# Kernel optimization log

Hardware: AMD Instinct MI355X
Metric: run time of the kernel (lower is better)

## Reference

```python
import jax, jax.numpy as jnp
import numpy as np

HEAD_SIZE = 128
EMBED_DIM = 1024
BLOCK = 2048


def setup_inputs() -> dict:
    key = jax.random.key(0)
    kx, kk, kq, kv = jax.random.split(key, 4)
    x = jax.random.normal(kx, (8, BLOCK, EMBED_DIM), dtype=jnp.float32)
    # nn.Linear weights stored as [out, in]; apply as x @ W.T -> keep as [in, out]
    s = 1.0 / np.sqrt(EMBED_DIM)
    W_key = jax.random.uniform(kk, (EMBED_DIM, HEAD_SIZE), jnp.float32, -s, s)
    W_query = jax.random.uniform(kq, (EMBED_DIM, HEAD_SIZE), jnp.float32, -s, s)
    W_value = jax.random.uniform(kv, (EMBED_DIM, HEAD_SIZE), jnp.float32, -s, s)
    return {"x": x, "W_key": W_key, "W_query": W_query, "W_value": W_value}


def reference(x, W_key, W_query, W_value):
    # NOTE: faithful to the source bug: q = self.key(x), W_query is unused.
    B, T, C = x.shape
    k = x @ W_key          # [B, T, H]
    q = x @ W_key          # [B, T, H]  (source uses key() for q too)
    scores = jnp.einsum("bqh,bkh->bqk", q, k) * (HEAD_SIZE ** -0.5)
    causal = jnp.tril(jnp.ones((T, T), dtype=bool))
    scores = jnp.where(causal, scores, -jnp.inf)
    weights = jax.nn.softmax(scores, axis=-1)
    v = x @ W_value        # [B, T, H]
    out = jnp.einsum("bqk,bkh->bqh", weights, v)
    return out
```

## Files before the change

kernel.cpp:

```cpp
#include <hip/hip_runtime.h>
#include <hip/hip_bf16.h>

typedef __attribute__((ext_vector_type(8))) short bf16x8;
typedef __attribute__((ext_vector_type(4))) short bf16x4;
typedef __attribute__((ext_vector_type(4))) float f32x4;

#define HS 128
#define ED 1024
#define TT 2048
#define NBATCH 8
#define NROWS (NBATCH * TT)
#define CHUNKS 4
#define TPC 8

__device__ __forceinline__ short bf16rne(float f) {
    unsigned u = __builtin_bit_cast(unsigned, f);
    u = u + 0x7fffu + ((u >> 16) & 1u);
    return (short)(u >> 16);
}

__device__ __forceinline__ void gl_lds16(const void* g, void* l) {
    __builtin_amdgcn_global_load_lds(
        (const __attribute__((address_space(1))) unsigned int*)g,
        (__attribute__((address_space(3))) unsigned int*)l, 16, 0, 0);
}

template <int NCALLS, int RBL2>
__device__ __forceinline__ void stage_tile(const char* gbase, void* lds,
                                           int gpitch, int tid, int wv) {
#pragma unroll
    for (int c = 0; c < NCALLS; ++c) {
        const int o = c * 4096 + tid * 16;
        const int row = o >> RBL2;
        const int colU = (o & ((1 << RBL2) - 1)) ^ ((row & 7) << 4);
        const char* g = gbase + (size_t)row * gpitch + colU;
        char* l = (char*)lds + c * 4096 + wv * 1024;
        gl_lds16(g, l);
    }
}

__device__ __forceinline__ bf16x8 lds_rd7(const short* lds, int row, int colE) {
    const int o = (row << 7) + (((colE * 2) & 127) ^ ((row & 7) << 4));
    return *reinterpret_cast<const bf16x8*>((const char*)lds + o);
}
__device__ __forceinline__ bf16x8 lds_rd8(const short* lds, int row, int colE) {
    const int o = (row << 8) + (((colE * 2) & 255) ^ ((row & 7) << 4));
    return *reinterpret_cast<const bf16x8*>((const char*)lds + o);
}

__global__ void k_wtrans(const float* __restrict__ Wk, const float* __restrict__ Wv,
                         short* __restrict__ WkT, short* __restrict__ WvT) {
    const float* W = blockIdx.y ? Wv : Wk;
    short* WT = blockIdx.y ? WvT : WkT;
    __shared__ float tile[16][128];
    const int k0 = blockIdx.x * 16;
    const int t = threadIdx.x;
#pragma unroll
    for (int i = 0; i < 8; ++i) {
        int idx = t + i * 256;
        tile[idx >> 7][idx & 127] = W[(size_t)(k0 + (idx >> 7)) * HS + (idx & 127)];
    }
    __syncthreads();
    const int n = t >> 1;
    const int h = (t & 1) * 8;
    bf16x8 o;
#pragma unroll
    for (int i = 0; i < 8; ++i) o[i] = bf16rne(tile[h + i][n]);
    *reinterpret_cast<bf16x8*>(&WT[(size_t)n * ED + k0 + h]) = o;
}

__global__ __launch_bounds__(256) void k_proj(
        const float* __restrict__ x,
        const short* __restrict__ WkT, const short* __restrict__ WvT,
        short* __restrict__ Kbuf, short* __restrict__ VT) {
    __shared__ short xl[2][64 * 64];
    __shared__ short wl[2][128 * 64];

    const int tid = threadIdx.x;
    const int lane = tid & 63;
    const int wv = tid >> 6;
    const int lr = lane & 15, g = lane >> 4;
    const int side = blockIdx.x;
    const int r0 = blockIdx.y * 64;
    const short* WT = side ? WvT : WkT;

    f32x4 acc[8];
#pragma unroll
    for (int i = 0; i < 8; ++i) acc[i] = (f32x4){0.f, 0.f, 0.f, 0.f};

    int xo[2], xrow[2], xcolU[2];
#pragma unroll
    for (int j = 0; j < 2; ++j) {
        xo[j] = tid * 32 + j * 16;
        xrow[j] = xo[j] >> 7;
        xcolU[j] = (xo[j] & 127) ^ ((xrow[j] & 7) << 4);
    }
    f32x4 xr[2][2][2];

#define XLOAD(s, set)                                                                \
    {                                                                                \
        _Pragma("unroll") for (int j = 0; j < 2; ++j) {                              \
            const float* sp = x + (size_t)(r0 + xrow[j]) * ED + (s) * 64 + (xcolU[j] >> 1); \
            xr[set][j][0] = *reinterpret_cast<const f32x4*>(sp);                     \
            xr[set][j][1] = *reinterpret_cast<const f32x4*>(sp + 4);                 \
        }                                                                            \
    }
#define XWRITE(set, buf)                                                             \
    {                                                                                \
        _Pragma("unroll") for (int j = 0; j < 2; ++j) {                              \
            bf16x8 pk;                                                               \
            _Pragma("unroll") for (int i = 0; i < 8; ++i)                            \
                pk[i] = bf16rne(xr[set][j][i >> 2][i & 3]);                          \
            *reinterpret_cast<bf16x8*>((char*)&xl[buf][0] + xo[j]) = pk;             \
        }                                                                            \
    }

    XLOAD(0, 0);
    XLOAD(1, 1);
    stage_tile<4, 7>((const char*)WT, &wl[0][0], ED * 2, tid, wv);
    XWRITE(0, 0);
    __syncthreads();

#pragma unroll
    for (int s = 0; s < 16; ++s) {
        const int cur = s & 1;
        if (s + 1 < 16) {
            stage_tile<4, 7>((const char*)WT + (size_t)(s + 1) * 128, &wl[cur ^ 1][0],
                             ED * 2, tid, wv);
            XWRITE((s + 1) & 1, cur ^ 1);
        }
        if (s + 2 < 16) XLOAD(s + 2, cur);
        bf16x8 af[2];
#pragma unroll
        for (int ks = 0; ks < 2; ++ks)
            af[ks] = lds_rd7(&xl[cur][0], wv * 16 + lr, ks * 32 + g * 8);
#pragma unroll
        for (int ks = 0; ks < 2; ++ks)
#pragma unroll
            for (int nf = 0; nf < 8; ++nf) {
                bf16x8 bfr = lds_rd7(&wl[cur][0], nf * 16 + lr, ks * 32 + g * 8);
                acc[nf] = __builtin_amdgcn_mfma_f32_16x16x32_bf16(af[ks], bfr, acc[nf], 0, 0, 0);
            }
        __syncthreads();
    }
#undef XLOAD
#undef XWRITE

    const int mb = r0 + wv * 16 + 4 * g;
    if (side == 0) {
#pragma unroll
        for (int nf = 0; nf < 8; ++nf) {
            const int n = nf * 16 + lr;
#pragma unroll
            for (int r = 0; r < 4; ++r)
                Kbuf[(size_t)(mb + r) * HS + n] = bf16rne(acc[nf][r]);
        }
    } else {
        const int b = mb >> 11, tt = mb & (TT - 1);
#pragma unroll
        for (int nf = 0; nf < 8; ++nf) {
            const int n = nf * 16 + lr;
            bf16x4 o;
#pragma unroll
            for (int r = 0; r < 4; ++r) o[r] = bf16rne(acc[nf][r]);
            *reinterpret_cast<bf16x4*>(&VT[((size_t)b * HS + n) * TT + tt]) = o;
        }
    }
}

__global__ __launch_bounds__(256) void k_attn(
        const short* __restrict__ Kbuf, const short* __restrict__ VT,
        float* __restrict__ Opart, float* __restrict__ ml) {
    __shared__ short kl[2][64 * 128];
    __shared__ short vl[2][128 * 64];
    __shared__ short plds[4][16][72];

    const int tid = threadIdx.x;
    const int lane = tid & 63;
    const int wv = tid >> 6;
    const int lr = lane & 15, g = lane >> 4;

    const int bid = blockIdx.x;
    const int b = bid & 7;
    const int w = bid >> 3;
    int c, qt;
    if (w < 32)      { c = 0; qt = 31 - w; }
    else if (w < 56) { c = 1; qt = 31 - (w - 32); }
    else if (w < 72) { c = 2; qt = 31 - (w - 56); }
    else             { c = 3; qt = 31 - (w - 72); }
    const int t_begin = c * TPC;
    const int t_end = min(t_begin + TPC, qt + 1);

    const short* Kb = Kbuf + (size_t)b * TT * HS;
    const short* Vb = VT + (size_t)b * HS * TT;
    const int q0 = qt * 64 + wv * 16;

    bf16x8 qf[4];
#pragma unroll
    for (int ks = 0; ks < 4; ++ks)
        qf[ks] = *reinterpret_cast<const bf16x8*>(&Kb[(size_t)(q0 + lr) * HS + ks * 32 + g * 8]);

    stage_tile<4, 8>((const char*)(Kb + (size_t)t_begin * 64 * HS), &kl[0][0], HS * 2, tid, wv);
    stage_tile<4, 7>((const char*)(Vb + t_begin * 64), &vl[0][0], TT * 2, tid, wv);
    __syncthreads();

    float mrun = -1e30f, lrun = 0.f;
    f32x4 oacc[8];
#pragma unroll
    for (int i = 0; i < 8; ++i) oacc[i] = (f32x4){0.f, 0.f, 0.f, 0.f};

    const float c1 = 0.08838834764831845f * 1.4426950408889634f;
    const int qrow = q0 + lr;
    int cur = 0;

    for (int t = t_begin; t < t_end; ++t) {
        const int kv0 = t * 64;
        if (t + 1 < t_end) {
            stage_tile<4, 8>((const char*)(Kb + (size_t)(kv0 + 64) * HS), &kl[cur ^ 1][0],
                             HS * 2, tid, wv);
            stage_tile<4, 7>((const char*)(Vb + kv0 + 64), &vl[cur ^ 1][0], TT * 2, tid, wv);
        }

        f32x4 s[4];
#pragma unroll
        for (int i = 0; i < 4; ++i) s[i] = (f32x4){0.f, 0.f, 0.f, 0.f};
        __builtin_amdgcn_s_setprio(1);
#pragma unroll
        for (int ks = 0; ks < 4; ++ks) {
            bf16x8 kf[4];
#pragma unroll
            for (int mf = 0; mf < 4; ++mf)
                kf[mf] = lds_rd8(&kl[cur][0], mf * 16 + lr, ks * 32 + g * 8);
#pragma unroll
            for (int mf = 0; mf < 4; ++mf)
                s[mf] = __builtin_amdgcn_mfma_f32_16x16x32_bf16(kf[mf], qf[ks], s[mf], 0, 0, 0);
        }
        __builtin_amdgcn_s_setprio(0);

        float pv[4][4];
        float tmax = -1e30f;
#pragma unroll
        for (int mf = 0; mf < 4; ++mf)
#pragma unroll
            for (int r = 0; r < 4; ++r) {
                const int kv = kv0 + mf * 16 + 4 * g + r;
                float v = s[mf][r] * c1;
                v = (kv <= qrow) ? v : -1e30f;
                pv[mf][r] = v;
                tmax = fmaxf(tmax, v);
            }
        tmax = fmaxf(tmax, __shfl_xor(tmax, 16));
        tmax = fmaxf(tmax, __shfl_xor(tmax, 32));
        const float mnew = fmaxf(mrun, tmax);
        const float alpha = exp2f(mrun - mnew);
        mrun = mnew;
        float tsum = 0.f;
#pragma unroll
        for (int mf = 0; mf < 4; ++mf)
#pragma unroll
            for (int r = 0; r < 4; ++r) {
                const float p = exp2f(pv[mf][r] - mnew);
                pv[mf][r] = p;
                tsum += p;
            }
        tsum += __shfl_xor(tsum, 16);
        tsum += __shfl_xor(tsum, 32);
        lrun = lrun * alpha + tsum;
#pragma unroll
        for (int i = 0; i < 8; ++i) oacc[i] *= alpha;

#pragma unroll
        for (int mf = 0; mf < 4; ++mf) {
            bf16x4 pk;
#pragma unroll
            for (int r = 0; r < 4; ++r) pk[r] = bf16rne(pv[mf][r]);
            *reinterpret_cast<bf16x4*>(&plds[wv][lr][mf * 16 + g * 4]) = pk;
        }
        __builtin_amdgcn_s_setprio(1);
#pragma unroll
        for (int ks = 0; ks < 2; ++ks) {
            bf16x8 pf = *reinterpret_cast<const bf16x8*>(&plds[wv][lr][ks * 32 + g * 8]);
            bf16x8 vf[8];
#pragma unroll
            for (int mf = 0; mf < 8; ++mf)
                vf[mf] = lds_rd7(&vl[cur][0], mf * 16 + lr, ks * 32 + g * 8);
#pragma unroll
            for (int mf = 0; mf < 8; ++mf)
                oacc[mf] = __builtin_amdgcn_mfma_f32_16x16x32_bf16(vf[mf], pf, oacc[mf], 0, 0, 0);
        }
        __builtin_amdgcn_s_setprio(0);

        __syncthreads();
        cur ^= 1;
    }

    const int row = b * TT + q0 + lr;
    const size_t pidx = (size_t)c * NROWS + row;
    float* op = Opart + pidx * HS;
#pragma unroll
    for (int mf = 0; mf < 8; ++mf)
        *reinterpret_cast<f32x4*>(&op[mf * 16 + g * 4]) = oacc[mf];
    if (lane < 16) {
        ml[pidx * 2] = mrun;
        ml[pidx * 2 + 1] = lrun;
    }
}

__global__ __launch_bounds__(256) void k_merge(const float* __restrict__ Opart,
                                               const float* __restrict__ ml,
                                               float* __restrict__ out) {
    const int idx = blockIdx.x * 256 + threadIdx.x;
    const int row = idx >> 5;
    const int h4 = (idx & 31) * 4;
    const int qt64 = (row & (TT - 1)) >> 6;
    const int nvalid = (qt64 >> 3) + 1;
    float m[CHUNKS], l[CHUNKS];
    float M = -1e30f;
#pragma unroll
    for (int c = 0; c < CHUNKS; ++c) {
        const bool valid = c < nvalid;
        const size_t p = (size_t)c * NROWS + row;
        m[c] = valid ? ml[p * 2] : -1e30f;
        l[c] = valid ? ml[p * 2 + 1] : 0.f;
        M = fmaxf(M, m[c]);
    }
    float denom = 0.f;
    f32x4 o = (f32x4){0.f, 0.f, 0.f, 0.f};
#pragma unroll
    for (int c = 0; c < CHUNKS; ++c) {
        const bool valid = c < nvalid;
        const float wgt = valid ? exp2f(m[c] - M) : 0.f;
        denom += wgt * l[c];
        if (valid) {
            f32x4 p = *reinterpret_cast<const f32x4*>(
                &Opart[((size_t)c * NROWS + row) * HS + h4]);
            o += p * wgt;
        }
    }
    const float inv = 1.0f / denom;
    *reinterpret_cast<f32x4*>(&out[(size_t)row * HS + h4]) = o * inv;
}

extern "C" void kernel_launch(void* const* d_in, const int* in_sizes, int n_in,
                              void* d_out, int out_size, void* d_ws, size_t ws_size,
                              hipStream_t stream) {
    (void)in_sizes; (void)n_in; (void)out_size; (void)ws_size;
    const float* x  = (const float*)d_in[0];
    const float* Wk = (const float*)d_in[1];
    const float* Wv = (const float*)d_in[3];
    float* out = (float*)d_out;

    char* ws = (char*)d_ws;
    short* Kbuf = (short*)ws;
    short* VT   = (short*)(ws + (size_t)NROWS * HS * 2);
    short* WkT  = (short*)(ws + 2 * (size_t)NROWS * HS * 2);
    short* WvT  = WkT + (size_t)HS * ED;
    float* Opart = (float*)(WvT + (size_t)HS * ED);
    float* mlb   = Opart + (size_t)CHUNKS * NROWS * HS;

    hipLaunchKernelGGL(k_wtrans, dim3(64, 2), dim3(256), 0, stream, Wk, Wv, WkT, WvT);
    hipLaunchKernelGGL(k_proj, dim3(2, NROWS / 64), dim3(256), 0, stream, x, WkT, WvT, Kbuf, VT);
    hipLaunchKernelGGL(k_attn, dim3(640), dim3(256), 0, stream, Kbuf, VT, Opart, mlb);
    hipLaunchKernelGGL(k_merge, dim3(NROWS * 32 / 256), dim3(256), 0, stream, Opart, mlb, out);
}
```

Measured before the change: 165.3 us.

## Replace full syncthreads with partial vmcnt waits to keep prefetches in flight

Swaps __syncthreads in the projection and attention loops for explicit s_waitcnt vmcnt(N) plus s_barrier, so the next tile's global-to-LDS loads can stay outstanding while the current tile is computed. The projection loop moves the X register-to-LDS write after the MFMA block, and the attention loop issues the next K/V stage at the top of each iteration, then waits only for the current tile. This relies on hand-counted outstanding memory operations and on the compiler's ordering, so a wrong count would race.

```diff
diff --git a/kernel.cpp b/kernel.cpp
--- a/kernel.cpp
+++ b/kernel.cpp
@@ -17,6 +17,17 @@
     unsigned u = __builtin_bit_cast(unsigned, f);
     u = u + 0x7fffu + ((u >> 16) & 1u);
     return (short)(u >> 16);
+}
+
+template <int N>
+__device__ __forceinline__ void vmwait() {
+    if constexpr (N == 0)      asm volatile("s_waitcnt vmcnt(0)" ::: "memory");
+    else if constexpr (N == 4) asm volatile("s_waitcnt vmcnt(4)" ::: "memory");
+    else                       asm volatile("s_waitcnt vmcnt(8)" ::: "memory");
+}
+__device__ __forceinline__ void lds_barrier() {
+    asm volatile("s_waitcnt lgkmcnt(0)" ::: "memory");
+    __builtin_amdgcn_s_barrier();
 }
 
 __device__ __forceinline__ void gl_lds16(const void* g, void* l) {
@@ -118,30 +129,31 @@
     XLOAD(0, 0);
     XLOAD(1, 1);
     stage_tile<4, 7>((const char*)WT, &wl[0][0], ED * 2, tid, wv);
+    vmwait<0>();
     XWRITE(0, 0);
-    __syncthreads();
+    lds_barrier();
 
 #pragma unroll
     for (int s = 0; s < 16; ++s) {
-        const int cur = s & 1;
-        if (s + 1 < 16) {
-            stage_tile<4, 7>((const char*)WT + (size_t)(s + 1) * 128, &wl[cur ^ 1][0],
-                             ED * 2, tid, wv);
-            XWRITE((s + 1) & 1, cur ^ 1);
-        }
-        if (s + 2 < 16) XLOAD(s + 2, cur);
+        if (s + 1 < 16)
+            stage_tile<4, 7>((const char*)WT + (size_t)(s + 1) * 128,
+                             &wl[(s + 1) & 1][0], ED * 2, tid, wv);
+        if (s + 2 < 16) XLOAD(s + 2, s & 1);
         bf16x8 af[2];
 #pragma unroll
         for (int ks = 0; ks < 2; ++ks)
-            af[ks] = lds_rd7(&xl[cur][0], wv * 16 + lr, ks * 32 + g * 8);
+            af[ks] = lds_rd7(&xl[s & 1][0], wv * 16 + lr, ks * 32 + g * 8);
 #pragma unroll
         for (int ks = 0; ks < 2; ++ks)
 #pragma unroll
             for (int nf = 0; nf < 8; ++nf) {
-                bf16x8 bfr = lds_rd7(&wl[cur][0], nf * 16 + lr, ks * 32 + g * 8);
+                bf16x8 bfr = lds_rd7(&wl[s & 1][0], nf * 16 + lr, ks * 32 + g * 8);
                 acc[nf] = __builtin_amdgcn_mfma_f32_16x16x32_bf16(af[ks], bfr, acc[nf], 0, 0, 0);
             }
-        __syncthreads();
+        if (s + 2 < 16) vmwait<4>();
+        else            vmwait<0>();
+        if (s + 1 < 16) XWRITE((s + 1) & 1, (s + 1) & 1);
+        lds_barrier();
     }
 #undef XLOAD
 #undef XWRITE
@@ -202,7 +214,6 @@
 
     stage_tile<4, 8>((const char*)(Kb + (size_t)t_begin * 64 * HS), &kl[0][0], HS * 2, tid, wv);
     stage_tile<4, 7>((const char*)(Vb + t_begin * 64), &vl[0][0], TT * 2, tid, wv);
-    __syncthreads();
 
     float mrun = -1e30f, lrun = 0.f;
     f32x4 oacc[8];
@@ -211,16 +222,20 @@
 
     const float c1 = 0.08838834764831845f * 1.4426950408889634f;
     const int qrow = q0 + lr;
-    int cur = 0;
 
     for (int t = t_begin; t < t_end; ++t) {
+        const int bi = (t - t_begin) & 1;
+        if (t + 1 < t_end) {
+            stage_tile<4, 8>((const char*)(Kb + (size_t)(t + 1) * 64 * HS), &kl[bi ^ 1][0],
+                             HS * 2, tid, wv);
+            stage_tile<4, 7>((const char*)(Vb + (t + 1) * 64), &vl[bi ^ 1][0], TT * 2, tid, wv);
+            vmwait<8>();
+        } else {
+            vmwait<0>();
+        }
+        __builtin_amdgcn_s_barrier();
+
         const int kv0 = t * 64;
-        if (t + 1 < t_end) {
-            stage_tile<4, 8>((const char*)(Kb + (size_t)(kv0 + 64) * HS), &kl[cur ^ 1][0],
-                             HS * 2, tid, wv);
-            stage_tile<4, 7>((const char*)(Vb + kv0 + 64), &vl[cur ^ 1][0], TT * 2, tid, wv);
-        }
-
         f32x4 s[4];
 #pragma unroll
         for (int i = 0; i < 4; ++i) s[i] = (f32x4){0.f, 0.f, 0.f, 0.f};
@@ -230,7 +245,7 @@
             bf16x8 kf[4];
 #pragma unroll
             for (int mf = 0; mf < 4; ++mf)
-                kf[mf] = lds_rd8(&kl[cur][0], mf * 16 + lr, ks * 32 + g * 8);
+                kf[mf] = lds_rd8(&kl[bi][0], mf * 16 + lr, ks * 32 + g * 8);
 #pragma unroll
             for (int mf = 0; mf < 4; ++mf)
                 s[mf] = __builtin_amdgcn_mfma_f32_16x16x32_bf16(kf[mf], qf[ks], s[mf], 0, 0, 0);
@@ -283,15 +298,14 @@
             bf16x8 vf[8];
 #pragma unroll
             for (int mf = 0; mf < 8; ++mf)
-                vf[mf] = lds_rd7(&vl[cur][0], mf * 16 + lr, ks * 32 + g * 8);
+                vf[mf] = lds_rd7(&vl[bi][0], mf * 16 + lr, ks * 32 + g * 8);
 #pragma unroll
             for (int mf = 0; mf < 8; ++mf)
                 oacc[mf] = __builtin_amdgcn_mfma_f32_16x16x32_bf16(vf[mf], pf, oacc[mf], 0, 0, 0);
         }
         __builtin_amdgcn_s_setprio(0);
 
-        __syncthreads();
-        cur ^= 1;
+        lds_barrier();
     }
 
     const int row = b * TT + q0 + lr;
```

Measured after the change: 165.3 us. No clear change (-0.0%).
